# Performance work log

Hardware: AMD Instinct MI355X
Metric: run time of the kernel (lower is better)

## Reference

```python
import jax, jax.numpy as jnp
import numpy as np

N_NODES = 4096
N_SUBS = 1024
NUM_FEATURES = 128
HIDDEN = 512
NHEADS = 8
DHEAD = HIDDEN // NHEADS
NUM_LAYERS = 2
EDGE_PROB = 0.01
NEG_INF = -1e9


def _make_adj(key, n, p):
    a = (jax.random.uniform(key, (n, n)) < p).astype(jnp.float32)
    return jnp.maximum(a, jnp.eye(n, dtype=jnp.float32))  # self-loops


def setup_inputs() -> dict:
    key = jax.random.key(0)
    ks = jax.random.split(key, 12)
    x = jax.random.normal(ks[0], (N_NODES, NUM_FEATURES), dtype=jnp.float32)
    adj_node = _make_adj(ks[1], N_NODES, EDGE_PROB)
    adj_substation = _make_adj(ks[2], N_SUBS, 4 * EDGE_PROB)
    seg_ids = jnp.sort(jax.random.randint(ks[3], (N_NODES,), 0, N_SUBS, dtype=jnp.int32))
    s = 0.05
    lin_w = jax.random.normal(ks[4], (NUM_FEATURES, HIDDEN), dtype=jnp.float32) * s
    lin_b = jnp.zeros((HIDDEN,), dtype=jnp.float32)
    node_W = jax.random.normal(ks[5], (NUM_LAYERS, HIDDEN, HIDDEN), dtype=jnp.float32) * s
    node_asrc = jax.random.normal(ks[6], (NUM_LAYERS, NHEADS, DHEAD), dtype=jnp.float32) * s
    node_adst = jax.random.normal(ks[7], (NUM_LAYERS, NHEADS, DHEAD), dtype=jnp.float32) * s
    sub_W = jax.random.normal(ks[8], (NUM_LAYERS, HIDDEN, HIDDEN), dtype=jnp.float32) * s
    sub_asrc = jax.random.normal(ks[9], (NUM_LAYERS, NHEADS, DHEAD), dtype=jnp.float32) * s
    sub_adst = jax.random.normal(ks[10], (NUM_LAYERS, NHEADS, DHEAD), dtype=jnp.float32) * s
    return {"x": x, "adj_node": adj_node, "adj_substation": adj_substation,
            "seg_ids": seg_ids, "lin_w": lin_w, "lin_b": lin_b,
            "node_W": node_W, "node_asrc": node_asrc, "node_adst": node_adst,
            "sub_W": sub_W, "sub_asrc": sub_asrc, "sub_adst": sub_adst}


def _gat_layer(h, adj, W, a_src, a_dst):
    # h: [N, F]; adj: [N, N]; W: [F, F]; a_src/a_dst: [H, Dh]
    n = h.shape[0]
    Wh = (h @ W).reshape(n, NHEADS, DHEAD)               # [N, H, Dh]
    f_src = jnp.einsum('nhd,hd->hn', Wh, a_src)          # [H, N]
    f_dst = jnp.einsum('nhd,hd->hn', Wh, a_dst)          # [H, N]
    e = jax.nn.leaky_relu(f_src[:, :, None] + f_dst[:, None, :], 0.2)  # [H, N, N]
    e = jnp.where(adj[None] > 0, e, NEG_INF)
    alpha = jax.nn.softmax(e, axis=-1)                   # [H, N, N]
    out = jnp.einsum('hij,jhd->ihd', alpha, Wh).reshape(n, NHEADS * DHEAD)
    return jax.nn.elu(out)


def _stacked_gats(h, adj, Ws, asrcs, adsts):
    # Faithful to the source bug: x is never rebound, each layer sees the
    # original input; the last layer's output is returned.
    out = h
    for i in range(Ws.shape[0]):
        out = _gat_layer(h, adj, Ws[i], asrcs[i], adsts[i])
    return out


def _pool_mean(h, seg_ids, num_segments):
    sums = jax.ops.segment_sum(h, seg_ids, num_segments=num_segments)
    counts = jax.ops.segment_sum(jnp.ones((h.shape[0], 1), h.dtype), seg_ids,
                                 num_segments=num_segments)
    return sums / jnp.maximum(counts, 1.0)


def reference(x, adj_node, adj_substation, seg_ids, lin_w, lin_b,
              node_W, node_asrc, node_adst, sub_W, sub_asrc, sub_adst):
    h = x @ lin_w + lin_b                                  # [N, HIDDEN]
    h = _stacked_gats(h, adj_node, node_W, node_asrc, node_adst)
    s = _pool_mean(h, seg_ids, N_SUBS)                     # [S, HIDDEN]
    s = _stacked_gats(s, adj_substation, sub_W, sub_asrc, sub_adst)
    return s
```

## Files before the change

kernel.cpp:

```cpp
#include <hip/hip_runtime.h>
#include <hip/hip_bf16.h>
#include <math.h>

#define N_NODES 4096
#define N_SUBS  1024
#define NFEAT   128
#define HIDDEN  512
#define NHEADS  8
#define DHEAD   64
#define CAP     128
#define ROWG    4

__global__ __launch_bounds__(256) void extract_ballot(const float* __restrict__ adj,
                                                      int N,
                                                      int* __restrict__ cnt,
                                                      int* __restrict__ nbr) {
    const int w = threadIdx.x >> 6;
    const int lane = threadIdx.x & 63;
    const int row = blockIdx.x * 4 + w;
    const float4* rowp = (const float4*)(adj + (size_t)row * N);
    int* nrow = nbr + (row << 7);
    const int n4 = N >> 2;
    int c = 0;
    const unsigned long long below = (1ull << lane) - 1ull;
    for (int c4 = lane; c4 < n4; c4 += 64) {
        const float4 v = rowp[c4];
        const int col = c4 << 2;
        unsigned long long m;
        bool p;
        p = v.x > 0.0f; m = __ballot(p);
        if (p) { int q = c + __popcll(m & below); if (q < CAP) nrow[q] = col; }
        c += __popcll(m);
        p = v.y > 0.0f; m = __ballot(p);
        if (p) { int q = c + __popcll(m & below); if (q < CAP) nrow[q] = col + 1; }
        c += __popcll(m);
        p = v.z > 0.0f; m = __ballot(p);
        if (p) { int q = c + __popcll(m & below); if (q < CAP) nrow[q] = col + 2; }
        c += __popcll(m);
        p = v.w > 0.0f; m = __ballot(p);
        if (p) { int q = c + __popcll(m & below); if (q < CAP) nrow[q] = col + 3; }
        c += __popcll(m);
    }
    if (lane == 0) cnt[row] = c < CAP ? c : CAP;
}

#define BM 64
#define BN 64
#define BK 16
__global__ __launch_bounds__(256) void gemm_f32(const float* __restrict__ A,
                                                const float* __restrict__ B,
                                                const float* __restrict__ bias,
                                                float* __restrict__ C,
                                                int M, int N, int K, int k_chunk,
                                                const float* __restrict__ asrc,
                                                const float* __restrict__ adst,
                                                float* __restrict__ fs,
                                                float* __restrict__ fd) {
    __shared__ float As[BK][BM + 4];
    __shared__ float Bs[BK][BN + 4];
    const int tid = threadIdx.x;
    const int bm = blockIdx.y * BM;
    const int bn = blockIdx.x * BN;
    const int k_start = blockIdx.z * k_chunk;
    const int k_end = (k_start + k_chunk) < K ? (k_start + k_chunk) : K;
    float* Cw = C + (size_t)blockIdx.z * M * N;
    const int tr = tid >> 4;
    const int tc = tid & 15;
    const int am = tid >> 2;
    const int ak4 = (tid & 3) * 4;
    const int bk = tid >> 4;
    const int bn0 = (tid & 15) * 4;
    float acc[4][4] = {};
    for (int k0 = k_start; k0 < k_end; k0 += BK) {
        const float4 va = *(const float4*)&A[(size_t)(bm + am) * K + k0 + ak4];
        const float4 vb = *(const float4*)&B[(size_t)(k0 + bk) * N + bn + bn0];
        As[ak4 + 0][am] = va.x;
        As[ak4 + 1][am] = va.y;
        As[ak4 + 2][am] = va.z;
        As[ak4 + 3][am] = va.w;
        *(float4*)&Bs[bk][bn0] = vb;
        __syncthreads();
#pragma unroll
        for (int k = 0; k < BK; k++) {
            const float4 a4 = *(const float4*)&As[k][tr * 4];
            const float4 b4 = *(const float4*)&Bs[k][tc * 4];
            const float a[4] = {a4.x, a4.y, a4.z, a4.w};
            const float b[4] = {b4.x, b4.y, b4.z, b4.w};
#pragma unroll
            for (int i = 0; i < 4; i++)
#pragma unroll
                for (int j = 0; j < 4; j++)
                    acc[i][j] += a[i] * b[j];
        }
        __syncthreads();
    }
#pragma unroll
    for (int i = 0; i < 4; i++) {
        const int m = bm + tr * 4 + i;
        if (bias) {
            const float4 bv = *(const float4*)&bias[bn + tc * 4];
            acc[i][0] += bv.x; acc[i][1] += bv.y; acc[i][2] += bv.z; acc[i][3] += bv.w;
        }
        float4 o = {acc[i][0], acc[i][1], acc[i][2], acc[i][3]};
        *(float4*)&Cw[(size_t)m * N + bn + tc * 4] = o;
    }
    if (asrc) {
        const int h = blockIdx.x;
        const float4 as4 = *(const float4*)&asrc[h * DHEAD + tc * 4];
        const float4 ad4 = *(const float4*)&adst[h * DHEAD + tc * 4];
#pragma unroll
        for (int i = 0; i < 4; i++) {
            float vs = acc[i][0] * as4.x + acc[i][1] * as4.y +
                       acc[i][2] * as4.z + acc[i][3] * as4.w;
            float vd = acc[i][0] * ad4.x + acc[i][1] * ad4.y +
                       acc[i][2] * ad4.z + acc[i][3] * ad4.w;
#pragma unroll
            for (int off = 1; off < 16; off <<= 1) {
                vs += __shfl_xor(vs, off, 64);
                vd += __shfl_xor(vd, off, 64);
            }
            if (tc == 0) {
                const int m = bm + tr * 4 + i;
                fs[h * M + m] = vs;
                fd[h * M + m] = vd;
            }
        }
    }
}

__global__ __launch_bounds__(256) void reduce_partials(const float* __restrict__ part,
                                                       float* __restrict__ outp,
                                                       int len, int nz) {
    int i = blockIdx.x * 256 + threadIdx.x;
    if (i < len) {
        float s = 0.0f;
        for (int z = 0; z < nz; z++) s += part[(size_t)z * len + i];
        outp[i] = s;
    }
}

__global__ __launch_bounds__(256) void gemv_bias_part(const float* __restrict__ lin_b,
                                                      const float* __restrict__ W1,
                                                      float* __restrict__ part) {
    const int n = blockIdx.x * 256 + threadIdx.x;
    const int z = blockIdx.y;
    const int k0 = z * (HIDDEN / 16);
    float s = 0.0f;
#pragma unroll 4
    for (int k = k0; k < k0 + HIDDEN / 16; k++)
        s += lin_b[k] * W1[(size_t)k * HIDDEN + n];
    part[z * HIDDEN + n] = s;
}

__global__ __launch_bounds__(512) void reduce_fsfd(const float* __restrict__ part,
                                                   float* __restrict__ wh,
                                                   const float* __restrict__ asrc,
                                                   const float* __restrict__ adst,
                                                   float* __restrict__ fs,
                                                   float* __restrict__ fd,
                                                   int M, int nz) {
    const int n = blockIdx.x;
    const int tid = threadIdx.x;
    float v = 0.0f;
    for (int z = 0; z < nz; z++)
        v += part[((size_t)z * M + n) * HIDDEN + tid];
    wh[(size_t)n * HIDDEN + tid] = v;
    const int h = tid >> 6;
    const int d = tid & 63;
    float vs = v * asrc[h * DHEAD + d];
    float vd = v * adst[h * DHEAD + d];
#pragma unroll
    for (int off = 32; off >= 1; off >>= 1) {
        vs += __shfl_xor(vs, off, 64);
        vd += __shfl_xor(vd, off, 64);
    }
    if (d == 0) {
        fs[h * M + n] = vs;
        fd[h * M + n] = vd;
    }
}

__global__ __launch_bounds__(512) void gat_agg(const float* __restrict__ Wh,
                                               const float* __restrict__ fs,
                                               const float* __restrict__ fd,
                                               const int* __restrict__ cnt,
                                               const int* __restrict__ nbr,
                                               float* __restrict__ out, int N) {
    __shared__ int snbr[CAP];
    __shared__ float ex[NHEADS][CAP + 1];
    __shared__ float sacc[ROWG][HIDDEN];
    const int i = blockIdx.x;
    const int tid = threadIdx.x;
    int C = cnt[i];
    C = C < CAP ? C : CAP;
    for (int k = tid; k < C; k += 512) snbr[k] = nbr[(i << 7) + k];
    __syncthreads();
    {
        const int h = tid >> 6;
        const int lane = tid & 63;
        const float fsi = fs[h * N + i];
        const float* __restrict__ fdh = fd + h * N;
        float m = -1e30f;
        for (int k = lane; k < C; k += 64) {
            float e = fsi + fdh[snbr[k]];
            e = e > 0.0f ? e : 0.2f * e;
            ex[h][k] = e;
            m = fmaxf(m, e);
        }
#pragma unroll
        for (int off = 32; off >= 1; off >>= 1) m = fmaxf(m, __shfl_xor(m, off, 64));
        float ssum = 0.0f;
        for (int k = lane; k < C; k += 64) {
            float v = __expf(ex[h][k] - m);
            ex[h][k] = v;
            ssum += v;
        }
#pragma unroll
        for (int off = 32; off >= 1; off >>= 1) ssum += __shfl_xor(ssum, off, 64);
        const float inv = 1.0f / ssum;
        for (int k = lane; k < C; k += 64) ex[h][k] *= inv;
    }
    __syncthreads();
    const int g = tid >> 7;
    const int t = tid & 127;
    const int hh = t >> 4;
    float4 acc = {0.f, 0.f, 0.f, 0.f};
    int k = g;
    for (; k + ROWG < C; k += 2 * ROWG) {
        const int j0 = snbr[k];
        const int j1 = snbr[k + ROWG];
        const float a0 = ex[hh][k];
        const float a1 = ex[hh][k + ROWG];
        const float4 w0 = *(const float4*)&Wh[(size_t)j0 * HIDDEN + 4 * t];
        const float4 w1 = *(const float4*)&Wh[(size_t)j1 * HIDDEN + 4 * t];
        acc.x += a0 * w0.x + a1 * w1.x;
        acc.y += a0 * w0.y + a1 * w1.y;
        acc.z += a0 * w0.z + a1 * w1.z;
        acc.w += a0 * w0.w + a1 * w1.w;
    }
    if (k < C) {
        const int j0 = snbr[k];
        const float a0 = ex[hh][k];
        const float4 w0 = *(const float4*)&Wh[(size_t)j0 * HIDDEN + 4 * t];
        acc.x += a0 * w0.x; acc.y += a0 * w0.y;
        acc.z += a0 * w0.z; acc.w += a0 * w0.w;
    }
    *(float4*)&sacc[g][4 * t] = acc;
    __syncthreads();
    if (g == 0) {
        float4 r = acc;
#pragma unroll
        for (int gg = 1; gg < ROWG; gg++) {
            const float4 o = *(const float4*)&sacc[gg][4 * t];
            r.x += o.x; r.y += o.y; r.z += o.z; r.w += o.w;
        }
        r.x = r.x > 0.0f ? r.x : __expf(r.x) - 1.0f;
        r.y = r.y > 0.0f ? r.y : __expf(r.y) - 1.0f;
        r.z = r.z > 0.0f ? r.z : __expf(r.z) - 1.0f;
        r.w = r.w > 0.0f ? r.w : __expf(r.w) - 1.0f;
        *(float4*)&out[(size_t)i * HIDDEN + 4 * t] = r;
    }
}

__global__ __launch_bounds__(512) void pool_kernel(const float* __restrict__ hin,
                                                   const int* __restrict__ seg,
                                                   float* __restrict__ sout) {
    const int s = blockIdx.x;
    const int d = threadIdx.x;
    int lo = 0, hi = N_NODES;
    while (lo < hi) { int mid = (lo + hi) >> 1; if (seg[mid] < s) lo = mid + 1; else hi = mid; }
    const int start = lo;
    hi = N_NODES;
    while (lo < hi) { int mid = (lo + hi) >> 1; if (seg[mid] < s + 1) lo = mid + 1; else hi = mid; }
    const int end = lo;
    float acc = 0.0f;
    for (int r = start; r < end; r++) acc += hin[(size_t)r * HIDDEN + d];
    const int c = end - start;
    sout[(size_t)s * HIDDEN + d] = acc / (c > 0 ? (float)c : 1.0f);
}

extern "C" void kernel_launch(void* const* d_in, const int* in_sizes, int n_in,
                              void* d_out, int out_size, void* d_ws, size_t ws_size,
                              hipStream_t stream) {
    const float* x        = (const float*)d_in[0];
    const float* adj_node = (const float*)d_in[1];
    const float* adj_sub  = (const float*)d_in[2];
    const int*   seg_ids  = (const int*)d_in[3];
    const float* lin_w    = (const float*)d_in[4];
    const float* lin_b    = (const float*)d_in[5];
    const float* node_W1    = (const float*)d_in[6]  + HIDDEN * HIDDEN;
    const float* node_asrc1 = (const float*)d_in[7]  + NHEADS * DHEAD;
    const float* node_adst1 = (const float*)d_in[8]  + NHEADS * DHEAD;
    const float* sub_W1     = (const float*)d_in[9]  + HIDDEN * HIDDEN;
    const float* sub_asrc1  = (const float*)d_in[10] + NHEADS * DHEAD;
    const float* sub_adst1  = (const float*)d_in[11] + NHEADS * DHEAD;
    float* out = (float*)d_out;

    char* ws = (char*)d_ws;
    float* bufA  = (float*)(ws);
    float* bufB  = (float*)(ws + (size_t)8 * 1024 * 1024);
    float* fs_n  = (float*)(ws + (size_t)16 * 1024 * 1024);
    float* fd_n  = fs_n + NHEADS * N_NODES;
    float* fs_s  = fd_n + NHEADS * N_NODES;
    float* fd_s  = fs_s + NHEADS * N_SUBS;
    int*   cnt_n = (int*)(fd_s + NHEADS * N_SUBS);
    int*   cnt_s = cnt_n + N_NODES;
    int*   nbr_n = cnt_s + N_SUBS;
    int*   nbr_s = nbr_n + N_NODES * CAP;

    float* Wpart = bufB;
    float* Wfuse = bufB + 16 * NFEAT * HIDDEN;
    float* bpart = Wfuse + NFEAT * HIDDEN;
    float* bias2 = bpart + 16 * HIDDEN;
    float* wh_n  = bufA;
    float* gatom = bufB;
    float* sp    = bufA;
    float* Spart = bufB;
    float* wh_s  = bufA + (size_t)N_SUBS * HIDDEN;

    extract_ballot<<<N_NODES / 4, 256, 0, stream>>>(adj_node, N_NODES, cnt_n, nbr_n);
    extract_ballot<<<N_SUBS / 4, 256, 0, stream>>>(adj_sub, N_SUBS, cnt_s, nbr_s);
    gemm_f32<<<dim3(HIDDEN / BN, NFEAT / BM, 16), 256, 0, stream>>>(
        lin_w, node_W1, nullptr, Wpart, NFEAT, HIDDEN, HIDDEN, HIDDEN / 16,
        nullptr, nullptr, nullptr, nullptr);
    gemv_bias_part<<<dim3(HIDDEN / 256, 16), 256, 0, stream>>>(lin_b, node_W1, bpart);
    reduce_partials<<<NFEAT * HIDDEN / 256, 256, 0, stream>>>(
        Wpart, Wfuse, NFEAT * HIDDEN, 16);
    reduce_partials<<<HIDDEN / 256, 256, 0, stream>>>(bpart, bias2, HIDDEN, 16);
    gemm_f32<<<dim3(HIDDEN / BN, N_NODES / BM, 1), 256, 0, stream>>>(
        x, Wfuse, bias2, wh_n, N_NODES, HIDDEN, NFEAT, NFEAT,
        node_asrc1, node_adst1, fs_n, fd_n);
    gat_agg<<<N_NODES, 512, 0, stream>>>(wh_n, fs_n, fd_n, cnt_n, nbr_n,
                                         gatom, N_NODES);
    pool_kernel<<<N_SUBS, 512, 0, stream>>>(gatom, seg_ids, sp);
    gemm_f32<<<dim3(HIDDEN / BN, N_SUBS / BM, 4), 256, 0, stream>>>(
        sp, sub_W1, nullptr, Spart, N_SUBS, HIDDEN, HIDDEN, HIDDEN / 4,
        nullptr, nullptr, nullptr, nullptr);
    reduce_fsfd<<<N_SUBS, 512, 0, stream>>>(Spart, wh_s, sub_asrc1, sub_adst1,
                                            fs_s, fd_s, N_SUBS, 4);
    gat_agg<<<N_SUBS, 512, 0, stream>>>(wh_s, fs_s, fd_s, cnt_s, nbr_s,
                                        out, N_SUBS);
}
```

Baseline: 231.5 us.

## Split node GAT aggregation into two neighbor-range passes and merge small launches

```diff
diff --git a/kernel.cpp b/kernel.cpp
--- a/kernel.cpp
+++ b/kernel.cpp
@@ -11,13 +11,25 @@
 #define CAP     128
 #define ROWG    4
 
-__global__ __launch_bounds__(256) void extract_ballot(const float* __restrict__ adj,
-                                                      int N,
-                                                      int* __restrict__ cnt,
-                                                      int* __restrict__ nbr) {
+__global__ __launch_bounds__(256) void extract_both(const float* __restrict__ adj_n,
+                                                    const float* __restrict__ adj_s,
+                                                    int* __restrict__ cnt_n,
+                                                    int* __restrict__ nbr_n,
+                                                    int* __restrict__ cnt_s,
+                                                    int* __restrict__ nbr_s) {
     const int w = threadIdx.x >> 6;
     const int lane = threadIdx.x & 63;
-    const int row = blockIdx.x * 4 + w;
+    const float* adj;
+    int N, row;
+    int* cnt;
+    int* nbr;
+    if (blockIdx.x < N_NODES / 4) {
+        adj = adj_n; N = N_NODES; cnt = cnt_n; nbr = nbr_n;
+        row = blockIdx.x * 4 + w;
+    } else {
+        adj = adj_s; N = N_SUBS; cnt = cnt_s; nbr = nbr_s;
+        row = (blockIdx.x - N_NODES / 4) * 4 + w;
+    }
     const float4* rowp = (const float4*)(adj + (size_t)row * N);
     int* nrow = nbr + (row << 7);
     const int n4 = N >> 2;
@@ -128,14 +140,27 @@
     }
 }
 
-__global__ __launch_bounds__(256) void reduce_partials(const float* __restrict__ part,
-                                                       float* __restrict__ outp,
-                                                       int len, int nz) {
-    int i = blockIdx.x * 256 + threadIdx.x;
-    if (i < len) {
-        float s = 0.0f;
-        for (int z = 0; z < nz; z++) s += part[(size_t)z * len + i];
-        outp[i] = s;
+__global__ __launch_bounds__(256) void reduce_both(const float* __restrict__ p1,
+                                                   float* __restrict__ o1,
+                                                   int len1, int nz1,
+                                                   const float* __restrict__ p2,
+                                                   float* __restrict__ o2,
+                                                   int len2, int nz2,
+                                                   int blocks1) {
+    if ((int)blockIdx.x < blocks1) {
+        const int i = blockIdx.x * 256 + threadIdx.x;
+        if (i < len1) {
+            float s = 0.0f;
+            for (int z = 0; z < nz1; z++) s += p1[(size_t)z * len1 + i];
+            o1[i] = s;
+        }
+    } else {
+        const int i = (blockIdx.x - blocks1) * 256 + threadIdx.x;
+        if (i < len2) {
+            float s = 0.0f;
+            for (int z = 0; z < nz2; z++) s += p2[(size_t)z * len2 + i];
+            o2[i] = s;
+        }
     }
 }
 
@@ -185,7 +210,9 @@
                                                const float* __restrict__ fd,
                                                const int* __restrict__ cnt,
                                                const int* __restrict__ nbr,
-                                               float* __restrict__ out, int N) {
+                                               float* __restrict__ out, int N,
+                                               int jlo, int jhi,
+                                               int first, int last) {
     __shared__ int snbr[CAP];
     __shared__ float ex[NHEADS][CAP + 1];
     __shared__ float sacc[ROWG][HIDDEN];
@@ -195,6 +222,8 @@
     C = C < CAP ? C : CAP;
     for (int k = tid; k < C; k += 512) snbr[k] = nbr[(i << 7) + k];
     __syncthreads();
+    const int klo = __syncthreads_count((tid < C) && (snbr[tid] < jlo));
+    const int khi = __syncthreads_count((tid < C) && (snbr[tid] < jhi));
     {
         const int h = tid >> 6;
         const int lane = tid & 63;
@@ -225,8 +254,8 @@
     const int t = tid & 127;
     const int hh = t >> 4;
     float4 acc = {0.f, 0.f, 0.f, 0.f};
-    int k = g;
-    for (; k + ROWG < C; k += 2 * ROWG) {
+    int k = klo + g;
+    for (; k + ROWG < khi; k += 2 * ROWG) {
         const int j0 = snbr[k];
         const int j1 = snbr[k + ROWG];
         const float a0 = ex[hh][k];
@@ -238,7 +267,7 @@
         acc.z += a0 * w0.z + a1 * w1.z;
         acc.w += a0 * w0.w + a1 * w1.w;
     }
-    if (k < C) {
+    if (k < khi) {
         const int j0 = snbr[k];
         const float a0 = ex[hh][k];
         const float4 w0 = *(const float4*)&Wh[(size_t)j0 * HIDDEN + 4 * t];
@@ -254,11 +283,18 @@
             const float4 o = *(const float4*)&sacc[gg][4 * t];
             r.x += o.x; r.y += o.y; r.z += o.z; r.w += o.w;
         }
-        r.x = r.x > 0.0f ? r.x : __expf(r.x) - 1.0f;
-        r.y = r.y > 0.0f ? r.y : __expf(r.y) - 1.0f;
-        r.z = r.z > 0.0f ? r.z : __expf(r.z) - 1.0f;
-        r.w = r.w > 0.0f ? r.w : __expf(r.w) - 1.0f;
-        *(float4*)&out[(size_t)i * HIDDEN + 4 * t] = r;
+        float4* op = (float4*)&out[(size_t)i * HIDDEN + 4 * t];
+        if (!first) {
+            const float4 p = *op;
+            r.x += p.x; r.y += p.y; r.z += p.z; r.w += p.w;
+        }
+        if (last) {
+            r.x = r.x > 0.0f ? r.x : __expf(r.x) - 1.0f;
+            r.y = r.y > 0.0f ? r.y : __expf(r.y) - 1.0f;
+            r.z = r.z > 0.0f ? r.z : __expf(r.z) - 1.0f;
+            r.w = r.w > 0.0f ? r.w : __expf(r.w) - 1.0f;
+        }
+        *op = r;
     }
 }
 
@@ -318,20 +354,22 @@
     float* Spart = bufB;
     float* wh_s  = bufA + (size_t)N_SUBS * HIDDEN;
 
-    extract_ballot<<<N_NODES / 4, 256, 0, stream>>>(adj_node, N_NODES, cnt_n, nbr_n);
-    extract_ballot<<<N_SUBS / 4, 256, 0, stream>>>(adj_sub, N_SUBS, cnt_s, nbr_s);
+    extract_both<<<N_NODES / 4 + N_SUBS / 4, 256, 0, stream>>>(
+        adj_node, adj_sub, cnt_n, nbr_n, cnt_s, nbr_s);
     gemm_f32<<<dim3(HIDDEN / BN, NFEAT / BM, 16), 256, 0, stream>>>(
         lin_w, node_W1, nullptr, Wpart, NFEAT, HIDDEN, HIDDEN, HIDDEN / 16,
         nullptr, nullptr, nullptr, nullptr);
     gemv_bias_part<<<dim3(HIDDEN / 256, 16), 256, 0, stream>>>(lin_b, node_W1, bpart);
-    reduce_partials<<<NFEAT * HIDDEN / 256, 256, 0, stream>>>(
-        Wpart, Wfuse, NFEAT * HIDDEN, 16);
-    reduce_partials<<<HIDDEN / 256, 256, 0, stream>>>(bpart, bias2, HIDDEN, 16);
+    reduce_both<<<NFEAT * HIDDEN / 256 + 2, 256, 0, stream>>>(
+        Wpart, Wfuse, NFEAT * HIDDEN, 16, bpart, bias2, HIDDEN, 16,
+        NFEAT * HIDDEN / 256);
     gemm_f32<<<dim3(HIDDEN / BN, N_NODES / BM, 1), 256, 0, stream>>>(
         x, Wfuse, bias2, wh_n, N_NODES, HIDDEN, NFEAT, NFEAT,
         node_asrc1, node_adst1, fs_n, fd_n);
     gat_agg<<<N_NODES, 512, 0, stream>>>(wh_n, fs_n, fd_n, cnt_n, nbr_n,
-                                         gatom, N_NODES);
+                                         gatom, N_NODES, 0, N_NODES / 2, 1, 0);
+    gat_agg<<<N_NODES, 512, 0, stream>>>(wh_n, fs_n, fd_n, cnt_n, nbr_n,
+                                         gatom, N_NODES, N_NODES / 2, N_NODES, 0, 1);
     pool_kernel<<<N_SUBS, 512, 0, stream>>>(gatom, seg_ids, sp);
     gemm_f32<<<dim3(HIDDEN / BN, N_SUBS / BM, 4), 256, 0, stream>>>(
         sp, sub_W1, nullptr, Spart, N_SUBS, HIDDEN, HIDDEN, HIDDEN / 4,
@@ -339,5 +377,5 @@
     reduce_fsfd<<<N_SUBS, 512, 0, stream>>>(Spart, wh_s, sub_asrc1, sub_adst1,
                                             fs_s, fd_s, N_SUBS, 4);
     gat_agg<<<N_SUBS, 512, 0, stream>>>(wh_s, fs_s, fd_s, cnt_s, nbr_s,
-                                        out, N_SUBS);
-}
+                                        out, N_SUBS, 0, N_SUBS, 1, 1);
+}
```

New measurement: 232.1 us. Within noise of the previous version (+0.2%).
